# Optimization experiments

Measured on AMD Instinct MI355X. Metric: run time of the kernel, lower is better.

Reference implementation:

```python
import jax, jax.numpy as jnp
import numpy as np

B, N, S, NS = 16, 4096, 512, 32
RADIUS = 0.4
EPS = 1e-5
CHANS = [6, 64, 64, 128]


def setup_inputs() -> dict:
    key = jax.random.key(0)
    ks = jax.random.split(key, 8)
    inp = {
        "xyz": jax.random.normal(ks[0], (B, 3, N), jnp.float32),
        "points": jax.random.normal(ks[1], (B, 3, N), jnp.float32),
    }
    for i in range(3):
        cin, cout = CHANS[i], CHANS[i + 1]
        inp[f"w{i}"] = jax.random.normal(ks[2 + i], (cout, cin), jnp.float32) * (1.0 / np.sqrt(cin))
        inp[f"b{i}"] = jnp.zeros((cout,), jnp.float32)
        inp[f"g{i}"] = jnp.ones((cout,), jnp.float32)
        inp[f"beta{i}"] = jnp.zeros((cout,), jnp.float32)
    return inp


def _fps(xyz):
    # xyz: [B, N, 3] -> indices [B, S] (deterministic start at index 0)
    n = xyz.shape[1]

    def step(carry, _):
        dist, far = carry
        centroid = jnp.take_along_axis(xyz, far[:, None, None], axis=1)  # [B,1,3]
        d = jnp.sum((xyz - centroid) ** 2, -1)                           # [B,N]
        dist = jnp.minimum(dist, d)
        nxt = jnp.argmax(dist, axis=-1).astype(jnp.int32)
        return (dist, nxt), far

    init = (jnp.full((xyz.shape[0], n), 1e10, xyz.dtype), jnp.zeros((xyz.shape[0],), jnp.int32))
    _, idx = jax.lax.scan(step, init, None, length=S)
    return idx.T  # [B, S]


def _query_ball(xyz, new_xyz):
    # xyz: [B,N,3], new_xyz: [B,S,3] -> group indices [B,S,NS]
    n = xyz.shape[1]
    sqr = (jnp.sum(new_xyz ** 2, -1)[:, :, None]
           + jnp.sum(xyz ** 2, -1)[:, None, :]
           - 2.0 * jnp.einsum('bsc,bnc->bsn', new_xyz, xyz))  # [B,S,N]
    grp = jnp.where(sqr <= RADIUS ** 2, jnp.arange(n, dtype=jnp.int32)[None, None, :], n)
    grp = jnp.sort(grp, axis=-1)[:, :, :NS]
    first = grp[:, :, :1]
    return jnp.where(grp == n, first, grp)


_gather = jax.vmap(lambda p, i: p[i])  # p:[N,C], i:[S,NS] -> [S,NS,C]


def _forward(xyz, points, params):
    xyz_t = jnp.transpose(xyz, (0, 2, 1))      # [B,N,3]
    pts_t = jnp.transpose(points, (0, 2, 1))   # [B,N,D]
    fps_idx = _fps(xyz_t)                      # [B,S]
    new_xyz = jnp.take_along_axis(xyz_t, fps_idx[:, :, None], axis=1)  # [B,S,3]
    grp = _query_ball(xyz_t, new_xyz)          # [B,S,NS]
    grouped_xyz = _gather(xyz_t, grp) - new_xyz[:, :, None, :]         # [B,S,NS,3]
    grouped_pts = _gather(pts_t, grp)          # [B,S,NS,D]
    feat = jnp.concatenate([grouped_xyz, grouped_pts], axis=-1)        # [B,S,NS,3+D]
    x = jnp.transpose(feat, (0, 3, 2, 1))      # [B,C,NS,S]
    for (w, b, g, beta) in params:
        x = jnp.einsum('oc,bcns->bons', w, x) + b[None, :, None, None]
        mean = jnp.mean(x, axis=(0, 2, 3), keepdims=True)
        var = jnp.mean((x - mean) ** 2, axis=(0, 2, 3), keepdims=True)
        x = (x - mean) * jax.lax.rsqrt(var + EPS)
        x = jax.nn.relu(x * g[None, :, None, None] + beta[None, :, None, None])
    new_points = jnp.max(x, axis=2)            # [B, C_out, S]
    return jnp.transpose(new_xyz, (0, 2, 1)), new_points


def reference(xyz, points, w0, b0, g0, beta0, w1, b1, g1, beta1, w2, b2, g2, beta2):
    params = [(w0, b0, g0, beta0), (w1, b1, g1, beta1), (w2, b2, g2, beta2)]
    return _forward(xyz, points, params)
```

## Files before the change

### kernel.cpp

```cpp
#include <hip/hip_runtime.h>
#include <math.h>

#define BB 16
#define NN 4096
#define SS 512
#define KK 32
#define NPIX (BB*SS*KK)
#define NGRP (BB*SS)

static constexpr float R2F  = (float)0.16000000000000003;
static constexpr float EPSF = 1e-5f;

constexpr size_t OFF_NXYZ = 0;
constexpr size_t OFF_GRP  = 98304;
constexpr size_t OFF_P1   = 98304 + 1048576;
constexpr size_t OFF_P2   = OFF_P1 + 32768;
constexpr size_t OFF_P3   = OFF_P2 + 32768;
constexpr size_t OFF_MR1  = OFF_P3 + 65536;
constexpr size_t OFF_MR2  = OFF_MR1 + 512;
constexpr size_t OFF_MR3  = OFF_MR2 + 512;
constexpr size_t OFF_Z3   = 2*1024*1024;
constexpr size_t Z3SZ     = (size_t)NPIX*128*4;
constexpr size_t OFF_Z2   = OFF_Z3 + Z3SZ;
constexpr size_t Z2SZ     = (size_t)NPIX*64*4;
constexpr size_t NEED_Z3  = OFF_Z3 + Z3SZ;
constexpr size_t NEED_Z2  = OFF_Z2 + Z2SZ;

#define DPP_U64MAX(key, ctrl) {                                                  \
    unsigned _hi = (unsigned)((key) >> 32), _lo = (unsigned)(key);               \
    unsigned _h2 = (unsigned)__builtin_amdgcn_update_dpp((int)_hi,(int)_hi,(ctrl),0xf,0xf,false); \
    unsigned _l2 = (unsigned)__builtin_amdgcn_update_dpp((int)_lo,(int)_lo,(ctrl),0xf,0xf,false); \
    unsigned long long _o = ((unsigned long long)_h2 << 32) | _l2;               \
    (key) = (_o > (key)) ? _o : (key); }

__global__ __launch_bounds__(512) void fps_kernel(const float* __restrict__ xyz,
        float* __restrict__ out0, float* __restrict__ nxyz, double* __restrict__ pzero){
  const int b = blockIdx.x;
  const float* xb = xyz + (size_t)b*3*NN;
  __shared__ float4 pt4[NN];
  __shared__ __align__(16) unsigned long long skey[2][8];
  __shared__ int hist[SS];
  const int t = threadIdx.x;
  const int lane = t & 63, wv = t >> 6;
  for (int i = b*512 + t; i < 16384; i += 16*512) pzero[i] = 0.0;
  float rx[8], ry[8], rz[8], rd[8];
#pragma unroll
  for (int j=0;j<8;j++){
    int i = t + 512*j;
    float x = xb[i], y = xb[NN+i], z = xb[2*NN+i];
    rx[j]=x; ry[j]=y; rz[j]=z;
    pt4[i] = make_float4(x,y,z,0.0f);
    rd[j]=1e10f;
  }
  __syncthreads();
  int far = 0;
  for (int s=0;s<SS;s++){
    const int buf = s & 1;
    float4 c = pt4[far];
    if (t==0) hist[s] = far;
    float bv = -1.0f; int bi = 0;
#pragma unroll
    for (int j=0;j<8;j++){
      float dx=__fsub_rn(rx[j],c.x), dy=__fsub_rn(ry[j],c.y), dz=__fsub_rn(rz[j],c.z);
      float d2=__fadd_rn(__fadd_rn(__fmul_rn(dx,dx),__fmul_rn(dy,dy)),__fmul_rn(dz,dz));
      float nd=fminf(rd[j],d2);
      rd[j]=nd;
      if (nd>bv){bv=nd;bi=t+512*j;}
    }
    unsigned long long key = ((unsigned long long)(unsigned)__float_as_int(bv) << 32)
                           | (unsigned)(~(unsigned)bi);
    DPP_U64MAX(key,0x111); DPP_U64MAX(key,0x112); DPP_U64MAX(key,0x114);
    DPP_U64MAX(key,0x118); DPP_U64MAX(key,0x142); DPP_U64MAX(key,0x143);
    if (lane==63) skey[buf][wv] = key;
    __syncthreads();
    unsigned long long k0=skey[buf][0], k1=skey[buf][1], k2=skey[buf][2], k3=skey[buf][3];
    unsigned long long k4=skey[buf][4], k5=skey[buf][5], k6=skey[buf][6], k7=skey[buf][7];
    unsigned long long m01=(k0>k1)?k0:k1, m23=(k2>k3)?k2:k3;
    unsigned long long m45=(k4>k5)?k4:k5, m67=(k6>k7)?k6:k7;
    unsigned long long mA=(m01>m23)?m01:m23, mB=(m45>m67)?m45:m67;
    unsigned long long m =(mA>mB)?mA:mB;
    far = (int)(~(unsigned)(m & 0xFFFFFFFFull));
  }
  __syncthreads();
  {
    int idx = hist[t];
    float4 c = pt4[idx];
    int gid = b*SS + t;
    nxyz[gid*3+0]=c.x; nxyz[gid*3+1]=c.y; nxyz[gid*3+2]=c.z;
    out0[(b*3+0)*SS+t]=c.x; out0[(b*3+1)*SS+t]=c.y; out0[(b*3+2)*SS+t]=c.z;
  }
}

__global__ __launch_bounds__(256) void ball_kernel(const float* __restrict__ xyz,
        const float* __restrict__ nxyz, int* __restrict__ grp){
  const int gw   = (blockIdx.x*256 + threadIdx.x) >> 6;
  const int lane = threadIdx.x & 63;
  if (gw >= NGRP) return;
  const int b = gw / SS;
  const float* xb = xyz + (size_t)b*3*NN;
  const float nx=nxyz[gw*3+0], ny=nxyz[gw*3+1], nz=nxyz[gw*3+2];
  const float sn = __fadd_rn(__fadd_rn(__fmul_rn(nx,nx),__fmul_rn(ny,ny)),__fmul_rn(nz,nz));
  int cnt=0, first=-1;
  int* g = grp + (size_t)gw*KK;
  for (int c=0;c<NN/64 && cnt<KK;c++){
    int i=c*64+lane;
    float x=xb[i], y=xb[NN+i], z=xb[2*NN+i];
    float sxx=__fadd_rn(__fadd_rn(__fmul_rn(x,x),__fmul_rn(y,y)),__fmul_rn(z,z));
    float dot=__fadd_rn(__fadd_rn(__fmul_rn(nx,x),__fmul_rn(ny,y)),__fmul_rn(nz,z));
    float sqr=__fsub_rn(__fadd_rn(sn,sxx),__fmul_rn(2.0f,dot));
    bool m = (sqr <= R2F);
    unsigned long long mask = __ballot(m);
    if (m){
      int pos = cnt + __popcll(mask & ((1ull<<lane)-1ull));
      if (pos < KK) g[pos] = i;
    }
    if (first<0 && mask) first = c*64 + (__ffsll((long long)mask) - 1);
    cnt += __popcll(mask);
  }
  if (cnt < KK && lane >= cnt && lane < KK) g[lane] = first;
}

__global__ void finalize_kernel(const double* __restrict__ part, float* __restrict__ mr, int C){
  int o = threadIdx.x;
  if (o < C){
    double s1=0.0, s2=0.0;
    for (int k=0;k<32;k++){ s1 += part[o*32+k]; s2 += part[(C+o)*32+k]; }
    const double n = (double)NPIX;
    double mean = s1/n;
    double var  = s2/n - mean*mean;
    mr[2*o]   = (float)mean;
    mr[2*o+1] = (float)(1.0/sqrt(var + (double)EPSF));
  }
}

constexpr int XIN = 0;
constexpr int W0F = 408;
constexpr int B0F = 792;
constexpr int W1F = 856;
constexpr int B1F = 4952;
constexpr int XBF = 5016;
constexpr int SRF = 9368;
constexpr int W2F = 9624;
constexpr int B2F = 17816;
constexpr int SM_SMALL = 9624;
constexpr int SM_BIG   = 17944;

template<int STAGE, bool STZ3, bool Z2IO>
__global__ __launch_bounds__(256,2) void mlp_kernel(
    const float* __restrict__ xyz, const float* __restrict__ pts,
    const float* __restrict__ nxyz, const int* __restrict__ grp,
    const float* __restrict__ w0, const float* __restrict__ b0,
    const float* __restrict__ mr1, const float* __restrict__ g0, const float* __restrict__ be0,
    const float* __restrict__ w1, const float* __restrict__ b1,
    const float* __restrict__ mr2, const float* __restrict__ g1, const float* __restrict__ be1,
    const float* __restrict__ w2, const float* __restrict__ b2,
    const float* __restrict__ mr3, const float* __restrict__ g2, const float* __restrict__ be2,
    double* __restrict__ part, float* __restrict__ out1,
    float* __restrict__ z2w, float* __restrict__ z3w)
{
  __shared__ float sm[(STAGE>=3)? SM_BIG : SM_SMALL];
  const int t   = threadIdx.x;
  const int blk = blockIdx.x;
  const int tx  = t & 15, ty = t >> 4;
  const int p0  = blk*64;
  const int slot = blk & 31;
  constexpr bool SKIP12 = (STAGE==3 && Z2IO);

  sm[SRF + t] = 0.0f;

  if constexpr (!SKIP12){
    for (int i=t;i<384;i+=256){ int o=i/6, c=i-o*6; sm[W0F + c*64 + o] = w0[i]; }
    if (t<64) sm[B0F+t] = b0[t];
    if constexpr (STAGE>=2){
      for (int i=t;i<4096;i+=256){ int o=i&63, c=i>>6; sm[W1F + c*64 + o] = w1[o*64+c]; }
      if (t<64) sm[B1F+t] = b1[t];
    }
    for (int i=t;i<384;i+=256){
      int c=i>>6, px=i&63, p=p0+px, gid=p>>5, bb=p>>14;
      int idx = grp[p];
      float v;
      if (c<3) v = __fsub_rn(xyz[(size_t)bb*3*NN + c*NN + idx], nxyz[gid*3+c]);
      else     v = pts[(size_t)bb*3*NN + (c-3)*NN + idx];
      sm[XIN + c*68 + px] = v;
    }
  }
  if constexpr (STAGE>=3){
    for (int i=t;i<8192;i+=256){ int o=i&127, c=i>>7; sm[W2F + c*128 + o] = w2[o*64+c]; }
    if (t<128) sm[B2F+t] = b2[t];
  }
  __syncthreads();

  float z[4][4];
  if constexpr (SKIP12){
#pragma unroll
    for (int i=0;i<4;i++){
      float4 v = *(const float4*)&z2w[(size_t)(p0 + ty*4 + i)*64 + tx*4];
      z[i][0]=v.x; z[i][1]=v.y; z[i][2]=v.z; z[i][3]=v.w;
    }
  } else {
#pragma unroll
    for (int i=0;i<4;i++)
#pragma unroll
      for (int j=0;j<4;j++) z[i][j]=0.0f;
#pragma unroll
    for (int k=0;k<6;k++){
      float4 xv = *(const float4*)&sm[XIN + k*68 + ty*4];
      float4 wv = *(const float4*)&sm[W0F + k*64 + tx*4];
      const float xs[4]={xv.x,xv.y,xv.z,xv.w};
      const float wsv[4]={wv.x,wv.y,wv.z,wv.w};
#pragma unroll
      for (int i=0;i<4;i++)
#pragma unroll
        for (int j=0;j<4;j++) z[i][j] = fmaf(xs[i], wsv[j], z[i][j]);
    }
#pragma unroll
    for (int i=0;i<4;i++)
#pragma unroll
      for (int j=0;j<4;j++) z[i][j] = __fadd_rn(z[i][j], sm[B0F + tx*4 + j]);

    if constexpr (STAGE==1){
#pragma unroll
      for (int j=0;j<4;j++){
        float s1=0.0f, s2=0.0f;
#pragma unroll
        for (int i=0;i<4;i++){ s1 = __fadd_rn(s1, z[i][j]); s2 = fmaf(z[i][j], z[i][j], s2); }
        atomicAdd(&sm[SRF + (tx*4+j)*2    ], s1);
        atomicAdd(&sm[SRF + (tx*4+j)*2 + 1], s2);
      }
      __syncthreads();
      if (t<128){ int ch=t>>1, m=t&1;
        atomicAdd(part + (size_t)((m? 64+ch : ch)*32 + slot), (double)sm[SRF+t]);
      }
      return;
    }

#pragma unroll
    for (int j=0;j<4;j++){
      int ch = tx*4+j;
      float m=mr1[2*ch], r=mr1[2*ch+1], gg=g0[ch], bt=be0[ch];
      float4 o;
      o.x = fmaxf(fmaf(__fmul_rn(__fsub_rn(z[0][j],m),r), gg, bt), 0.0f);
      o.y = fmaxf(fmaf(__fmul_rn(__fsub_rn(z[1][j],m),r), gg, bt), 0.0f);
      o.z = fmaxf(fmaf(__fmul_rn(__fsub_rn(z[2][j],m),r), gg, bt), 0.0f);
      o.w = fmaxf(fmaf(__fmul_rn(__fsub_rn(z[3][j],m),r), gg, bt), 0.0f);
      *(float4*)&sm[XBF + ch*68 + ty*4] = o;
    }
    __syncthreads();

#pragma unroll
    for (int i=0;i<4;i++)
#pragma unroll
      for (int j=0;j<4;j++) z[i][j]=0.0f;
#pragma unroll 8
    for (int k=0;k<64;k++){
      float4 xv = *(const float4*)&sm[XBF + k*68 + ty*4];
      float4 wv = *(const float4*)&sm[W1F + k*64 + tx*4];
      const float xs[4]={xv.x,xv.y,xv.z,xv.w};
      const float wsv[4]={wv.x,wv.y,wv.z,wv.w};
#pragma unroll
      for (int i=0;i<4;i++)
#pragma unroll
        for (int j=0;j<4;j++) z[i][j] = fmaf(xs[i], wsv[j], z[i][j]);
    }
#pragma unroll
    for (int i=0;i<4;i++)
#pragma unroll
      for (int j=0;j<4;j++) z[i][j] = __fadd_rn(z[i][j], sm[B1F + tx*4 + j]);

    if constexpr (STAGE==2){
      if constexpr (Z2IO){
#pragma unroll
        for (int i=0;i<4;i++)
          *(float4*)&z2w[(size_t)(p0 + ty*4 + i)*64 + tx*4]
              = make_float4(z[i][0], z[i][1], z[i][2], z[i][3]);
      }
#pragma unroll
      for (int j=0;j<4;j++){
        float s1=0.0f, s2=0.0f;
#pragma unroll
        for (int i=0;i<4;i++){ s1 = __fadd_rn(s1, z[i][j]); s2 = fmaf(z[i][j], z[i][j], s2); }
        atomicAdd(&sm[SRF + (tx*4+j)*2    ], s1);
        atomicAdd(&sm[SRF + (tx*4+j)*2 + 1], s2);
      }
      __syncthreads();
      if (t<128){ int ch=t>>1, m=t&1;
        atomicAdd(part + (size_t)((m? 64+ch : ch)*32 + slot), (double)sm[SRF+t]);
      }
      return;
    }
  }

  if constexpr (STAGE>=3){
    __syncthreads();
#pragma unroll
    for (int j=0;j<4;j++){
      int ch = tx*4+j;
      float m=mr2[2*ch], r=mr2[2*ch+1], gg=g1[ch], bt=be1[ch];
      float4 o;
      o.x = fmaxf(fmaf(__fmul_rn(__fsub_rn(z[0][j],m),r), gg, bt), 0.0f);
      o.y = fmaxf(fmaf(__fmul_rn(__fsub_rn(z[1][j],m),r), gg, bt), 0.0f);
      o.z = fmaxf(fmaf(__fmul_rn(__fsub_rn(z[2][j],m),r), gg, bt), 0.0f);
      o.w = fmaxf(fmaf(__fmul_rn(__fsub_rn(z[3][j],m),r), gg, bt), 0.0f);
      *(float4*)&sm[XBF + ch*68 + ty*4] = o;
    }
    __syncthreads();

    float a3[4][8];
#pragma unroll
    for (int i=0;i<4;i++)
#pragma unroll
      for (int j=0;j<8;j++) a3[i][j]=0.0f;
#pragma unroll 4
    for (int k=0;k<64;k++){
      float4 xv  = *(const float4*)&sm[XBF + k*68  + ty*4];
      float4 wv0 = *(const float4*)&sm[W2F + k*128 + tx*4];
      float4 wv1 = *(const float4*)&sm[W2F + k*128 + 64 + tx*4];
      const float xs[4]={xv.x,xv.y,xv.z,xv.w};
      const float wsv[8]={wv0.x,wv0.y,wv0.z,wv0.w, wv1.x,wv1.y,wv1.z,wv1.w};
#pragma unroll
      for (int i=0;i<4;i++)
#pragma unroll
        for (int j=0;j<8;j++) a3[i][j] = fmaf(xs[i], wsv[j], a3[i][j]);
    }
#pragma unroll
    for (int i=0;i<4;i++)
#pragma unroll
      for (int j=0;j<8;j++){
        int ch = (j<4)? (tx*4+j) : (64+tx*4+(j-4));
        a3[i][j] = __fadd_rn(a3[i][j], sm[B2F + ch]);
      }

    if constexpr (STAGE==3){
      if constexpr (STZ3){
#pragma unroll
        for (int i=0;i<4;i++){
          size_t p = (size_t)(p0 + ty*4 + i)*128;
          *(float4*)&z3w[p + tx*4]      = make_float4(a3[i][0],a3[i][1],a3[i][2],a3[i][3]);
          *(float4*)&z3w[p + 64 + tx*4] = make_float4(a3[i][4],a3[i][5],a3[i][6],a3[i][7]);
        }
      }
#pragma unroll
      for (int j=0;j<8;j++){
        int ch = (j<4)? (tx*4+j) : (64+tx*4+(j-4));
        float s1=0.0f, s2=0.0f;
#pragma unroll
        for (int i=0;i<4;i++){ s1 = __fadd_rn(s1, a3[i][j]); s2 = fmaf(a3[i][j], a3[i][j], s2); }
        atomicAdd(&sm[SRF + ch*2    ], s1);
        atomicAdd(&sm[SRF + ch*2 + 1], s2);
      }
      __syncthreads();
      { int ch=t>>1, m=t&1;
        atomicAdd(part + (size_t)((m? 128+ch : ch)*32 + slot), (double)sm[SRF+t]);
      }
      return;
    }

    if constexpr (STAGE==4){
      const int grp_l = ty>>3;
      unsigned* omax = (unsigned*)sm;
#pragma unroll
      for (int j=0;j<8;j++){
        int ch = (j<4)? (tx*4+j) : (64+tx*4+(j-4));
        float m=mr3[2*ch], r=mr3[2*ch+1], gg=g2[ch], bt=be2[ch];
        float vmax=0.0f;
#pragma unroll
        for (int i=0;i<4;i++){
          float v = fmaxf(fmaf(__fmul_rn(__fsub_rn(a3[i][j],m),r), gg, bt), 0.0f);
          vmax = fmaxf(vmax, v);
        }
        atomicMax(&omax[SRF + grp_l*128 + ch], __float_as_uint(vmax));
      }
      __syncthreads();
      { int g = t>>7, o = t&127;
        int gid = blk*2 + g, bb = gid>>9, s = gid&511;
        out1[((size_t)(bb*128+o))*512 + s] = __uint_as_float(omax[SRF + t]);
      }
    }
  }
}

__global__ __launch_bounds__(256) void maxpool_kernel(const float* __restrict__ z3,
        const float* __restrict__ mr3, const float* __restrict__ g2,
        const float* __restrict__ be2, float* __restrict__ out1){
  const int t = threadIdx.x;
  const int g = blockIdx.x*2 + (t>>7);
  const int o = t & 127;
  const int bb = g >> 9, s = g & 511;
  const float* zp = z3 + (size_t)g*KK*128 + o;
  float m=mr3[2*o], r=mr3[2*o+1], gg=g2[o], bt=be2[o];
  float mx = 0.0f;
#pragma unroll 8
  for (int k=0;k<KK;k++){
    float v = fmaxf(fmaf(__fmul_rn(__fsub_rn(zp[(size_t)k*128],m),r), gg, bt), 0.0f);
    mx = fmaxf(mx, v);
  }
  out1[((size_t)(bb*128+o))*SS + s] = mx;
}

extern "C" void kernel_launch(void* const* d_in, const int* in_sizes, int n_in,
                              void* d_out, int out_size, void* d_ws, size_t ws_size,
                              hipStream_t stream){
  const float* xyz = (const float*)d_in[0];
  const float* pts = (const float*)d_in[1];
  const float* w0  = (const float*)d_in[2];  const float* b0  = (const float*)d_in[3];
  const float* g0  = (const float*)d_in[4];  const float* be0 = (const float*)d_in[5];
  const float* w1  = (const float*)d_in[6];  const float* b1  = (const float*)d_in[7];
  const float* g1  = (const float*)d_in[8];  const float* be1 = (const float*)d_in[9];
  const float* w2  = (const float*)d_in[10]; const float* b2  = (const float*)d_in[11];
  const float* g2  = (const float*)d_in[12]; const float* be2 = (const float*)d_in[13];

  float* out  = (float*)d_out;
  float* out1 = out + BB*3*SS;
  char*  ws   = (char*)d_ws;

  float*  nxyz = (float*)(ws + OFF_NXYZ);
  int*    grp  = (int*)  (ws + OFF_GRP);
  double* p1   = (double*)(ws + OFF_P1);
  double* p2   = (double*)(ws + OFF_P2);
  double* p3   = (double*)(ws + OFF_P3);
  float*  mr1  = (float*)(ws + OFF_MR1);
  float*  mr2  = (float*)(ws + OFF_MR2);
  float*  mr3  = (float*)(ws + OFF_MR3);
  float*  z3w  = (float*)(ws + OFF_Z3);
  float*  z2w  = (float*)(ws + OFF_Z2);

  const bool stz3 = (ws_size >= NEED_Z3);
  const bool stz2 = (ws_size >= NEED_Z2);

  fps_kernel <<<BB, 512, 0, stream>>>(xyz, out, nxyz, p1);
  ball_kernel<<<NGRP*64/256, 256, 0, stream>>>(xyz, nxyz, grp);

#define MLP_ARGS xyz, pts, nxyz, grp, w0, b0, mr1, g0, be0, w1, b1, mr2, g1, be1, w2, b2, mr3, g2, be2
  mlp_kernel<1,false,false><<<NPIX/64, 256, 0, stream>>>(MLP_ARGS, p1, out1, z2w, z3w);
  finalize_kernel<<<1,128,0,stream>>>(p1, mr1, 64);
  if (stz2) mlp_kernel<2,false,true ><<<NPIX/64, 256, 0, stream>>>(MLP_ARGS, p2, out1, z2w, z3w);
  else      mlp_kernel<2,false,false><<<NPIX/64, 256, 0, stream>>>(MLP_ARGS, p2, out1, z2w, z3w);
  finalize_kernel<<<1,128,0,stream>>>(p2, mr2, 64);
  if (stz2)      mlp_kernel<3,true ,true ><<<NPIX/64, 256, 0, stream>>>(MLP_ARGS, p3, out1, z2w, z3w);
  else if (stz3) mlp_kernel<3,true ,false><<<NPIX/64, 256, 0, stream>>>(MLP_ARGS, p3, out1, z2w, z3w);
  else           mlp_kernel<3,false,false><<<NPIX/64, 256, 0, stream>>>(MLP_ARGS, p3, out1, z2w, z3w);
  finalize_kernel<<<1,128,0,stream>>>(p3, mr3, 128);
  if (stz3) maxpool_kernel<<<NGRP/2, 256, 0, stream>>>(z3w, mr3, g2, be2, out1);
  else      mlp_kernel<4,false,false><<<NPIX/64, 256, 0, stream>>>(MLP_ARGS, p3, out1, z2w, z3w);
#undef MLP_ARGS
}
```

Measured before the change: 800.4 us.

## Replace stored layer-3 activations with per-group min/max for pooling

Stage 3 no longer writes the full 128-channel pre-norm activation tensor. For each group it keeps a per-channel max and min using order-preserving integer atomics in shared memory, then writes those to a small buffer. The pool kernel applies BN and ReLU to both extremes and takes the larger, which works because an affine map followed by ReLU is monotone in either direction depending on sign. This removes a large global write and re-read in exchange for extra shared atomics, and the workspace requirement is now smaller.

```diff
diff --git a/kernel.cpp b/kernel.cpp
--- a/kernel.cpp
+++ b/kernel.cpp
@@ -19,12 +19,11 @@
 constexpr size_t OFF_MR1  = OFF_P3 + 65536;
 constexpr size_t OFF_MR2  = OFF_MR1 + 512;
 constexpr size_t OFF_MR3  = OFF_MR2 + 512;
-constexpr size_t OFF_Z3   = 2*1024*1024;
-constexpr size_t Z3SZ     = (size_t)NPIX*128*4;
-constexpr size_t OFF_Z2   = OFF_Z3 + Z3SZ;
+constexpr size_t OFF_Z2   = 2*1024*1024;
 constexpr size_t Z2SZ     = (size_t)NPIX*64*4;
-constexpr size_t NEED_Z3  = OFF_Z3 + Z3SZ;
-constexpr size_t NEED_Z2  = OFF_Z2 + Z2SZ;
+constexpr size_t OFF_POOL = OFF_Z2 + Z2SZ;
+constexpr size_t POOLSZ   = (size_t)NGRP*256*4;
+constexpr size_t NEED_POOL= OFF_POOL + POOLSZ;
 
 #define DPP_U64MAX(key, ctrl) {                                                  \
     unsigned _hi = (unsigned)((key) >> 32), _lo = (unsigned)(key);               \
@@ -32,6 +31,14 @@
     unsigned _l2 = (unsigned)__builtin_amdgcn_update_dpp((int)_lo,(int)_lo,(ctrl),0xf,0xf,false); \
     unsigned long long _o = ((unsigned long long)_h2 << 32) | _l2;               \
     (key) = (_o > (key)) ? _o : (key); }
+
+__device__ __forceinline__ unsigned encf(float f){
+  unsigned u = __float_as_uint(f);
+  return u ^ (0x80000000u | (unsigned)((int)u >> 31));
+}
+__device__ __forceinline__ float decf(unsigned e){
+  return (e & 0x80000000u) ? __uint_as_float(e ^ 0x80000000u) : __uint_as_float(~e);
+}
 
 __global__ __launch_bounds__(512) void fps_kernel(const float* __restrict__ xyz,
         float* __restrict__ out0, float* __restrict__ nxyz, double* __restrict__ pzero){
@@ -142,10 +149,11 @@
 constexpr int SRF = 9368;
 constexpr int W2F = 9624;
 constexpr int B2F = 17816;
+constexpr int POOLU = 17944;
 constexpr int SM_SMALL = 9624;
-constexpr int SM_BIG   = 17944;
-
-template<int STAGE, bool STZ3, bool Z2IO>
+constexpr int SM_BIG   = 18456;
+
+template<int STAGE, bool POOL, bool Z2IO>
 __global__ __launch_bounds__(256,2) void mlp_kernel(
     const float* __restrict__ xyz, const float* __restrict__ pts,
     const float* __restrict__ nxyz, const int* __restrict__ grp,
@@ -156,7 +164,7 @@
     const float* __restrict__ w2, const float* __restrict__ b2,
     const float* __restrict__ mr3, const float* __restrict__ g2, const float* __restrict__ be2,
     double* __restrict__ part, float* __restrict__ out1,
-    float* __restrict__ z2w, float* __restrict__ z3w)
+    float* __restrict__ z2w, unsigned* __restrict__ poolg)
 {
   __shared__ float sm[(STAGE>=3)? SM_BIG : SM_SMALL];
   const int t   = threadIdx.x;
@@ -167,6 +175,11 @@
   constexpr bool SKIP12 = (STAGE==3 && Z2IO);
 
   sm[SRF + t] = 0.0f;
+  if constexpr (STAGE==3 && POOL){
+    unsigned* pu = (unsigned*)sm;
+    pu[POOLU + t]       = 0u;
+    pu[POOLU + 256 + t] = 0xFFFFFFFFu;
+  }
 
   if constexpr (!SKIP12){
     for (int i=t;i<384;i+=256){ int o=i/6, c=i-o*6; sm[W0F + c*64 + o] = w0[i]; }
@@ -331,12 +344,16 @@
       }
 
     if constexpr (STAGE==3){
-      if constexpr (STZ3){
-#pragma unroll
-        for (int i=0;i<4;i++){
-          size_t p = (size_t)(p0 + ty*4 + i)*128;
-          *(float4*)&z3w[p + tx*4]      = make_float4(a3[i][0],a3[i][1],a3[i][2],a3[i][3]);
-          *(float4*)&z3w[p + 64 + tx*4] = make_float4(a3[i][4],a3[i][5],a3[i][6],a3[i][7]);
+      if constexpr (POOL){
+        unsigned* pu = (unsigned*)sm;
+        const int gl = ty>>3;
+#pragma unroll
+        for (int j=0;j<8;j++){
+          int ch = (j<4)? (tx*4+j) : (64+tx*4+(j-4));
+          float mx = fmaxf(fmaxf(a3[0][j],a3[1][j]), fmaxf(a3[2][j],a3[3][j]));
+          float mn = fminf(fminf(a3[0][j],a3[1][j]), fminf(a3[2][j],a3[3][j]));
+          atomicMax(&pu[POOLU + gl*128 + ch], encf(mx));
+          atomicMin(&pu[POOLU + 256 + gl*128 + ch], encf(mn));
         }
       }
 #pragma unroll
@@ -351,6 +368,13 @@
       __syncthreads();
       { int ch=t>>1, m=t&1;
         atomicAdd(part + (size_t)((m? 128+ch : ch)*32 + slot), (double)sm[SRF+t]);
+      }
+      if constexpr (POOL){
+        unsigned* pu = (unsigned*)sm;
+        const int gl2 = t>>7, ch2 = t&127;
+        size_t base = (size_t)(blk*2+gl2)*256;
+        poolg[base + ch2]       = pu[POOLU + gl2*128 + ch2];
+        poolg[base + 128 + ch2] = pu[POOLU + 256 + gl2*128 + ch2];
       }
       return;
     }
@@ -379,22 +403,19 @@
   }
 }
 
-__global__ __launch_bounds__(256) void maxpool_kernel(const float* __restrict__ z3,
+__global__ __launch_bounds__(256) void pool_kernel(const unsigned* __restrict__ poolg,
         const float* __restrict__ mr3, const float* __restrict__ g2,
         const float* __restrict__ be2, float* __restrict__ out1){
   const int t = threadIdx.x;
-  const int g = blockIdx.x*2 + (t>>7);
-  const int o = t & 127;
-  const int bb = g >> 9, s = g & 511;
-  const float* zp = z3 + (size_t)g*KK*128 + o;
-  float m=mr3[2*o], r=mr3[2*o+1], gg=g2[o], bt=be2[o];
-  float mx = 0.0f;
-#pragma unroll 8
-  for (int k=0;k<KK;k++){
-    float v = fmaxf(fmaf(__fmul_rn(__fsub_rn(zp[(size_t)k*128],m),r), gg, bt), 0.0f);
-    mx = fmaxf(mx, v);
-  }
-  out1[((size_t)(bb*128+o))*SS + s] = mx;
+  const int gl = t>>7, ch = t&127;
+  const int gid = blockIdx.x*2 + gl;
+  const int bb = gid>>9, s = gid&511;
+  float fmx = decf(poolg[(size_t)gid*256 + ch]);
+  float fmn = decf(poolg[(size_t)gid*256 + 128 + ch]);
+  float m=mr3[2*ch], r=mr3[2*ch+1], gg=g2[ch], bt=be2[ch];
+  float ya = fmaxf(fmaf(__fmul_rn(__fsub_rn(fmx,m),r), gg, bt), 0.0f);
+  float yb = fmaxf(fmaf(__fmul_rn(__fsub_rn(fmn,m),r), gg, bt), 0.0f);
+  out1[((size_t)(bb*128+ch))*SS + s] = fmaxf(ya, yb);
 }
 
 extern "C" void kernel_launch(void* const* d_in, const int* in_sizes, int n_in,
@@ -413,34 +434,32 @@
   float* out1 = out + BB*3*SS;
   char*  ws   = (char*)d_ws;
 
-  float*  nxyz = (float*)(ws + OFF_NXYZ);
-  int*    grp  = (int*)  (ws + OFF_GRP);
-  double* p1   = (double*)(ws + OFF_P1);
-  double* p2   = (double*)(ws + OFF_P2);
-  double* p3   = (double*)(ws + OFF_P3);
-  float*  mr1  = (float*)(ws + OFF_MR1);
-  float*  mr2  = (float*)(ws + OFF_MR2);
-  float*  mr3  = (float*)(ws + OFF_MR3);
-  float*  z3w  = (float*)(ws + OFF_Z3);
-  float*  z2w  = (float*)(ws + OFF_Z2);
-
-  const bool stz3 = (ws_size >= NEED_Z3);
-  const bool stz2 = (ws_size >= NEED_Z2);
+  float*    nxyz  = (float*)(ws + OFF_NXYZ);
+  int*      grp   = (int*)  (ws + OFF_GRP);
+  double*   p1    = (double*)(ws + OFF_P1);
+  double*   p2    = (double*)(ws + OFF_P2);
+  double*   p3    = (double*)(ws + OFF_P3);
+  float*    mr1   = (float*)(ws + OFF_MR1);
+  float*    mr2   = (float*)(ws + OFF_MR2);
+  float*    mr3   = (float*)(ws + OFF_MR3);
+  float*    z2w   = (float*)(ws + OFF_Z2);
+  unsigned* poolg = (unsigned*)(ws + OFF_POOL);
+
+  const bool pool = (ws_size >= NEED_POOL);
 
   fps_kernel <<<BB, 512, 0, stream>>>(xyz, out, nxyz, p1);
   ball_kernel<<<NGRP*64/256, 256, 0, stream>>>(xyz, nxyz, grp);
 
 #define MLP_ARGS xyz, pts, nxyz, grp, w0, b0, mr1, g0, be0, w1, b1, mr2, g1, be1, w2, b2, mr3, g2, be2
-  mlp_kernel<1,false,false><<<NPIX/64, 256, 0, stream>>>(MLP_ARGS, p1, out1, z2w, z3w);
+  mlp_kernel<1,false,false><<<NPIX/64, 256, 0, stream>>>(MLP_ARGS, p1, out1, z2w, poolg);
   finalize_kernel<<<1,128,0,stream>>>(p1, mr1, 64);
-  if (stz2) mlp_kernel<2,false,true ><<<NPIX/64, 256, 0, stream>>>(MLP_ARGS, p2, out1, z2w, z3w);
-  else      mlp_kernel<2,false,false><<<NPIX/64, 256, 0, stream>>>(MLP_ARGS, p2, out1, z2w, z3w);
+  if (pool) mlp_kernel<2,false,true ><<<NPIX/64, 256, 0, stream>>>(MLP_ARGS, p2, out1, z2w, poolg);
+  else      mlp_kernel<2,false,false><<<NPIX/64, 256, 0, stream>>>(MLP_ARGS, p2, out1, z2w, poolg);
   finalize_kernel<<<1,128,0,stream>>>(p2, mr2, 64);
-  if (stz2)      mlp_kernel<3,true ,true ><<<NPIX/64, 256, 0, stream>>>(MLP_ARGS, p3, out1, z2w, z3w);
-  else if (stz3) mlp_kernel<3,true ,false><<<NPIX/64, 256, 0, stream>>>(MLP_ARGS, p3, out1, z2w, z3w);
-  else           mlp_kernel<3,false,false><<<NPIX/64, 256, 0, stream>>>(MLP_ARGS, p3, out1, z2w, z3w);
+  if (pool) mlp_kernel<3,true ,true ><<<NPIX/64, 256, 0, stream>>>(MLP_ARGS, p3, out1, z2w, poolg);
+  else      mlp_kernel<3,false,false><<<NPIX/64, 256, 0, stream>>>(MLP_ARGS, p3, out1, z2w, poolg);
   finalize_kernel<<<1,128,0,stream>>>(p3, mr3, 128);
-  if (stz3) maxpool_kernel<<<NGRP/2, 256, 0, stream>>>(z3w, mr3, g2, be2, out1);
-  else      mlp_kernel<4,false,false><<<NPIX/64, 256, 0, stream>>>(MLP_ARGS, p3, out1, z2w, z3w);
+  if (pool) pool_kernel<<<NGRP/2, 256, 0, stream>>>(poolg, mr3, g2, be2, out1);
+  else      mlp_kernel<4,false,false><<<NPIX/64, 256, 0, stream>>>(MLP_ARGS, p3, out1, z2w, poolg);
 #undef MLP_ARGS
 }
```

New measurement: 791.9 us. No clear change (-1.1%).
